# Optimization experiments

Measured on AMD Instinct MI355X. Metric: run time of the kernel, lower is better.

The kernel has to match this reference:

```python
import jax, jax.numpy as jnp
import numpy as np

B, C_IN, C_OUT, H, W = 4, 64, 64, 128, 128
N = 9  # 3x3 sampling points


def setup_inputs() -> dict:
    key = jax.random.key(0)
    k1, k2, k3, k4 = jax.random.split(key, 4)
    x = jax.random.normal(k1, (B, C_IN, H, W), jnp.float32)
    alpha = jax.random.normal(k2, (B, 1, H, W), jnp.float32)
    # kaiming_uniform(a=sqrt(5)) on (C_OUT, C_IN, 3, 3): bound = 1/sqrt(fan_in)
    fan_in = C_IN * 9
    bound = 1.0 / np.sqrt(fan_in)
    weight = jax.random.uniform(k3, (C_OUT, C_IN, 3, 3), jnp.float32, -bound, bound)
    bias = jax.random.uniform(k4, (C_OUT,), jnp.float32, -bound, bound)
    return {"x": x, "alpha": alpha, "weight": weight, "bias": bias}


def _forward(x, alpha, weight, bias):
    b, c, h, w = x.shape
    xp = jnp.pad(x, ((0, 0), (0, 0), (1, 1), (1, 1)))  # ZeroPad2d(1)
    hp, wp = h + 2, w + 2
    dt = x.dtype

    # kernel offsets, N index n = kx*3 + ky (kx slow)
    ks = jnp.arange(-1, 2, dtype=dt)
    pnx = jnp.repeat(ks, 3)  # [-1,-1,-1,0,0,0,1,1,1]
    pny = jnp.tile(ks, 3)    # [-1,0,1,-1,0,1,-1,0,1]

    cosA = jnp.cos(alpha)  # (b,1,h,w)
    sinA = jnp.sin(alpha)
    p0x = jnp.arange(1, h + 1, dtype=dt)[:, None]  # (h,1)
    p0y = jnp.arange(1, w + 1, dtype=dt)[None, :]  # (1,w)
    # note: original code multiplies each coord by (cos +/- sin) of alpha
    px = pnx[None, :, None, None] * (cosA + sinA) + p0x[None, None]  # (b,9,h,w)
    py = pny[None, :, None, None] * (cosA - sinA) + p0y[None, None]
    px = jnp.moveaxis(px, 1, -1)  # (b,h,w,9)
    py = jnp.moveaxis(py, 1, -1)

    fx, fy = jnp.floor(px), jnp.floor(py)  # detached in original (floor grad = 0)
    qx0 = jnp.clip(fx, 0, hp - 1)
    qx1 = jnp.clip(fx + 1, 0, hp - 1)
    qy0 = jnp.clip(fy, 0, wp - 1)
    qy1 = jnp.clip(fy + 1, 0, wp - 1)

    g_lt = (1 + (qx0 - px)) * (1 + (qy0 - py))
    g_rb = (1 - (qx1 - px)) * (1 - (qy1 - py))
    g_lb = (1 + (qx0 - px)) * (1 - (qy1 - py))
    g_rt = (1 - (qx1 - px)) * (1 + (qy0 - py))

    xf = xp.reshape(b, c, hp * wp)
    ix0, ix1 = qx0.astype(jnp.int32), qx1.astype(jnp.int32)
    iy0, iy1 = qy0.astype(jnp.int32), qy1.astype(jnp.int32)

    def gather(ix, iy):
        idx = (ix * wp + iy).reshape(b, -1)  # row-major flatten, like torch gather
        v = jax.vmap(lambda xb, ib: xb[:, ib])(xf, idx)  # (b,c,h*w*9)
        return v.reshape(b, c, h, w, N)

    emap = (g_lt[:, None] * gather(ix0, iy0)
            + g_rb[:, None] * gather(ix1, iy1)
            + g_lb[:, None] * gather(ix0, iy1)
            + g_rt[:, None] * gather(ix1, iy0))  # (b,c,h,w,9)

    # _reshape_x_offset: out[b,c, i*3+ky, j*3+kx] = emap[b,c,i,j, kx*3+ky]
    e = emap.reshape(b, c, h, w, 3, 3)              # (...,kx,ky)
    e = e.transpose(0, 1, 2, 5, 3, 4).reshape(b, c, 3 * h, 3 * w)

    # Dconv: central-difference weights, middle row = -(top + bottom)
    o, i = weight.shape[0], weight.shape[1]
    wr = weight.reshape(o, i, 9)
    r0, r2 = wr[:, :, 0:3], wr[:, :, 6:9]
    buf = jnp.concatenate([r0, -r0 - r2, r2], axis=-1).reshape(o, i, 3, 3)

    y = jax.lax.conv_general_dilated(
        e, buf, window_strides=(3, 3), padding='VALID',
        dimension_numbers=('NCHW', 'OIHW', 'NCHW'))
    return y + bias[None, :, None, None]


def reference(x, alpha, weight, bias):
    return _forward(x, alpha, weight, bias)
```

## Files before the change

### kernel.cpp

```cpp
#include <hip/hip_runtime.h>

#define CIN  64
#define COUT 64
#define Hn   128
#define Wn   128
#define HW   (Hn * Wn)
#define KDIM 576
#define WROW 1152
#define EROW 640

#define NRQ 5
#define NCQ 36
#define NCHUNKQ (NRQ * NCQ * 8)
#define TILE_BYTES (NCHUNKQ * 16)

typedef __attribute__((ext_vector_type(8))) short bf16x8;
typedef __attribute__((ext_vector_type(4))) float f32x4;
typedef __attribute__((ext_vector_type(2))) float f32x2;

__device__ __forceinline__ unsigned short f2bf(float f) {
    unsigned u = __float_as_uint(f);
    unsigned r = u + 0x7FFFu + ((u >> 16) & 1u);
    return (unsigned short)(r >> 16);
}
__device__ __forceinline__ unsigned pk2(float a, float b) {
    return (unsigned)f2bf(a) | ((unsigned)f2bf(b) << 16);
}
__device__ __forceinline__ unsigned pk2h(float a, float b) {
    unsigned ua = __float_as_uint(a) + 0x8000u;
    unsigned ub = __float_as_uint(b) + 0x8000u;
    return __builtin_amdgcn_perm(ub, ua, 0x07060302u);
}


__global__ __launch_bounds__(256) void prep_fused(
    const float* __restrict__ x, const float* __restrict__ weight,
    unsigned short* __restrict__ xt, unsigned short* __restrict__ Wtb2)
{
    __shared__ float fbuf[64][65];
    if (blockIdx.x >= 1024) {
        int e = (blockIdx.x - 1024) * 256 + threadIdx.x;
        if (e < COUT * KDIM) {
            int o = e / KDIM, k = e % KDIM;
            int n = k >> 6, c = k & 63;
            int u = n % 3, v = n / 3;
            float w0 = weight[((o * CIN + c) * 3 + 0) * 3 + v];
            float w2 = weight[((o * CIN + c) * 3 + 2) * 3 + v];
            float val = (u == 0) ? w0 : ((u == 1) ? (-w0 - w2) : w2);
            int s = c >> 5;
            int ce = c & 31;
            Wtb2[((n * 2 + s) * 64 + o) * 32 + ce] = f2bf(val);
        }
        return;
    }
    const int blk = blockIdx.x;
    const int b   = blk >> 8;
    const int rem = blk & 255;
    const int h   = rem >> 1;
    const int w0  = (rem & 1) << 6;
    const int t   = threadIdx.x;
    {
        int wq = t & 63, cq = t >> 6;
        const float* xp = x + ((size_t)(b * CIN + cq * 16) * Hn + h) * Wn + w0 + wq;
        #pragma unroll
        for (int r = 0; r < 16; ++r)
            fbuf[wq][cq * 16 + r] = xp[(size_t)r * HW];
    }
    __syncthreads();
    {
        int wq = t >> 2, q = t & 3;
        const float* row = &fbuf[wq][q * 16];
        uint4 d0, d1;
        d0.x = pk2(row[0],  row[1]);  d0.y = pk2(row[2],  row[3]);
        d0.z = pk2(row[4],  row[5]);  d0.w = pk2(row[6],  row[7]);
        d1.x = pk2(row[8],  row[9]);  d1.y = pk2(row[10], row[11]);
        d1.z = pk2(row[12], row[13]); d1.w = pk2(row[14], row[15]);
        unsigned short* op = xt + ((size_t)(b * Hn + h) * Wn + w0 + wq) * 64 + q * 16;
        *reinterpret_cast<uint4*>(op)     = d0;
        *reinterpret_cast<uint4*>(op + 8) = d1;
    }
}

template<int D>
__device__ __forceinline__ void axis_pts(float s, int base1, int org,
                                         int& l0, int& l1, float& w0, float& w1)
{
    if (D) {
        float p  = (float)D * s + (float)base1;
        float f  = floorf(p);
        float q0 = fminf(fmaxf(f,       0.f), 129.f);
        float q1 = fminf(fmaxf(f + 1.f, 0.f), 129.f);
        w0 = 1.f + (q0 - p);  w1 = 1.f - (q1 - p);
        int i0 = (int)q0, i1 = (int)q1;
        if (i0 < 1 || i0 > 128) w0 = 0.f;
        if (i1 < 1 || i1 > 128) w1 = 0.f;
        l0 = min(max(i0 - 1, 0), 127) - org;
        l1 = min(max(i1 - 1, 0), 127) - org;
    } else {
        l0 = base1 - 1 - org;  w0 = 1.f;
        l1 = l0;               w1 = 0.f;
    }
}

__device__ __forceinline__ void mkpt(int lr, int lc, int g16,
                                     unsigned& offL, unsigned& offH) {
    unsigned base = (unsigned)((lr * NCQ + lc) << 7);
    unsigned m    = ((unsigned)lc & 7u) << 4;
    offL = base + (((unsigned)g16) ^ m);
    offH = base + (((unsigned)(64 + g16)) ^ m);
}

template<int DX, int DY>
__device__ __forceinline__ void geoC(float s1, float s2, int i, int j0, int lpx,
        int g16, unsigned oL[4], unsigned oH[4], float gw[4])
{
    int r0, r1, c0, c1; float wx0, wx1, wy0, wy1;
    axis_pts<DX>(s1, i + 1,        i - 2,  r0, r1, wx0, wx1);
    axis_pts<DY>(s2, j0 + lpx + 1, j0 - 2, c0, c1, wy0, wy1);
    mkpt(r0, c0, g16, oL[0], oH[0]);  gw[0] = wx0 * wy0;
    mkpt(r0, c1, g16, oL[1], oH[1]);  gw[1] = wx0 * wy1;
    mkpt(r1, c0, g16, oL[2], oH[2]);  gw[2] = wx1 * wy0;
    mkpt(r1, c1, g16, oL[3], oH[3]);  gw[3] = wx1 * wy1;
}

template<int DX, int DY>
__device__ __forceinline__ void geoE(float s1, float s2, int i, int j0, int lpx,
        int g16, unsigned oL[2], unsigned oH[2], float gw[2])
{
    if (DX == 0) {
        int c0, c1; float wy0, wy1;
        axis_pts<DY>(s2, j0 + lpx + 1, j0 - 2, c0, c1, wy0, wy1);
        mkpt(2, c0, g16, oL[0], oH[0]);  gw[0] = wy0;
        mkpt(2, c1, g16, oL[1], oH[1]);  gw[1] = wy1;
    } else {
        int r0, r1; float wx0, wx1;
        axis_pts<DX>(s1, i + 1, i - 2, r0, r1, wx0, wx1);
        mkpt(r0, lpx + 2, g16, oL[0], oH[0]);  gw[0] = wx0;
        mkpt(r1, lpx + 2, g16, oL[1], oH[1]);  gw[1] = wx1;
    }
}

__device__ __forceinline__ f32x2 bfpair(unsigned u) {
    f32x2 r;
    r.x = __uint_as_float(u << 16);
    r.y = __uint_as_float(u & 0xFFFF0000u);
    return r;
}

__device__ __forceinline__ void fma16p(uint4 rl, uint4 rh, float gw,
                                       f32x2* v0, f32x2* v1) {
    const unsigned* u0 = reinterpret_cast<const unsigned*>(&rl);
    const unsigned* u1 = reinterpret_cast<const unsigned*>(&rh);
    f32x2 g2; g2.x = gw; g2.y = gw;
    #pragma unroll
    for (int q = 0; q < 4; ++q) {
        v0[q] = __builtin_elementwise_fma(g2, bfpair(u0[q]), v0[q]);
        v1[q] = __builtin_elementwise_fma(g2, bfpair(u1[q]), v1[q]);
    }
}

__device__ __forceinline__ bf16x8 packv2(const f32x2* v) {
    uint4 p;
    p.x = pk2h(v[0].x, v[0].y); p.y = pk2h(v[1].x, v[1].y);
    p.z = pk2h(v[2].x, v[2].y); p.w = pk2h(v[3].x, v[3].y);
    union { uint4 u; bf16x8 b; } cv; cv.u = p;
    return cv.b;
}

__global__ __launch_bounds__(256, 3) void ddconv_ws3(
    const unsigned short* __restrict__ xt, const float* __restrict__ alpha,
    const unsigned short* __restrict__ Wtb2, const float* __restrict__ bias,
    float* __restrict__ out)
{
    __shared__ __align__(16) char smem[40960];

    const int blk  = blockIdx.x;
    const int b    = blk >> 9;
    const int rem  = blk & 511;
    const int i    = rem >> 2;
    const int j0   = (rem & 3) << 5;
    const int t    = threadIdx.x;
    const int lane = t & 63;
    const int w    = t >> 6;
    const int llo  = lane & 15;
    const int g    = lane >> 4;
    const int g16  = g * 16;

    const char* xtb = (const char*)xt + (size_t)b * HW * 128;
    const char* wt2 = (const char*)Wtb2;
    const int arow  = llo * 64 + g16;

    char* tile = smem;
    uint4    sv[6];
    unsigned sla[6];
    {
        const char* sgp[6];
        #pragma unroll
        for (int k = 0; k < 6; ++k) {
            int q = t + k * 256;
            if (k == 5) q = min(q, NCHUNKQ - 1);
            int slot = q & 7;
            int rc   = q >> 3;
            int row  = rc / NCQ;
            int col  = rc - row * NCQ;
            int ru   = min(max(i - 2 + row, 0), 127);
            int cu   = min(max(j0 - 2 + col, 0), 127);
            sgp[k] = xtb + (size_t)(((ru << 7) + cu) << 7) + (slot << 4);
            sla[k] = ((unsigned)rc << 7) + (((unsigned)slot << 4) ^ (((unsigned)col & 7u) << 4));
        }
        #pragma unroll
        for (int k = 0; k < 6; ++k)
            sv[k] = *reinterpret_cast<const uint4*>(sgp[k]);
    }
    #pragma unroll
    for (int k = 0; k < 5; ++k)
        *reinterpret_cast<uint4*>(tile + sla[k]) = sv[k];
    if (t < NCHUNKQ - 5 * 256)
        *reinterpret_cast<uint4*>(tile + sla[5]) = sv[5];

    const int nn0 = (w==0)?0:(w==1)?2:(w==2)?6:8;
    const int nn1 = (w==0)?1:(w==1)?3:(w==2)?7:5;
    const int cs  = w >> 1;
    bf16x8 Ata[2][4], Atb[2][4], Ac0, Ac1;
    #pragma unroll
    for (int s = 0; s < 2; ++s)
      #pragma unroll
      for (int ot = 0; ot < 4; ++ot) {
        Ata[s][ot] = *reinterpret_cast<const bf16x8*>(wt2 + (nn0*2+s)*4096 + ot*1024 + arow);
        Atb[s][ot] = *reinterpret_cast<const bf16x8*>(wt2 + (nn1*2+s)*4096 + ot*1024 + arow);
      }
    Ac0 = *reinterpret_cast<const bf16x8*>(wt2 + (8+cs)*4096 + ((w&1)*2  )*1024 + arow);
    Ac1 = *reinterpret_cast<const bf16x8*>(wt2 + (8+cs)*4096 + ((w&1)*2+1)*1024 + arow);

    float* sAB = reinterpret_cast<float*>(smem + TILE_BYTES);
    if (t < 32) {
        float a = alpha[(b * Hn + i) * Wn + j0 + t];
        float sa, ca;
        sincosf(a, &sa, &ca);
        sAB[t]      = ca + sa;
        sAB[32 + t] = ca - sa;
    }

    f32x4 acc[2][4];
    #pragma unroll
    for (int pg = 0; pg < 2; ++pg)
      #pragma unroll
      for (int ot = 0; ot < 4; ++ot) acc[pg][ot] = (f32x4){0.f, 0.f, 0.f, 0.f};

    __syncthreads();

    float S1[2], S2[2];
    #pragma unroll
    for (int pg = 0; pg < 2; ++pg) {
        S1[pg] = sAB[pg * 16 + llo];
        S2[pg] = sAB[32 + pg * 16 + llo];
    }

    #pragma unroll
    for (int pg = 0; pg < 2; ++pg) {
        const int lpx = pg * 16 + llo;

        unsigned AL[4], AH[4], BL[2], BH[2];
        float    AG[4], BG[2];
        if (w == 0) {
            geoC<-1,-1>(S1[pg], S2[pg], i, j0, lpx, g16, AL, AH, AG);
            geoE<-1, 0>(S1[pg], S2[pg], i, j0, lpx, g16, BL, BH, BG);
        } else if (w == 1) {
            geoC<-1, 1>(S1[pg], S2[pg], i, j0, lpx, g16, AL, AH, AG);
            geoE< 0,-1>(S1[pg], S2[pg], i, j0, lpx, g16, BL, BH, BG);
        } else if (w == 2) {
            geoC< 1,-1>(S1[pg], S2[pg], i, j0, lpx, g16, AL, AH, AG);
            geoE< 1, 0>(S1[pg], S2[pg], i, j0, lpx, g16, BL, BH, BG);
        } else {
            geoC< 1, 1>(S1[pg], S2[pg], i, j0, lpx, g16, AL, AH, AG);
            geoE< 0, 1>(S1[pg], S2[pg], i, j0, lpx, g16, BL, BH, BG);
        }
        unsigned cb    = (unsigned)((2 * NCQ + lpx + 2) << 7);
        unsigned cm    = ((unsigned)(lpx + 2) & 7u) << 4;
        unsigned cAddr = cb + ((cs ? (unsigned)(64 + g16) : (unsigned)g16) ^ cm);

        uint4 La[4], Ha[4];
        #pragma unroll
        for (int p = 0; p < 4; ++p) {
            La[p] = *reinterpret_cast<const uint4*>(tile + AL[p]);
            Ha[p] = *reinterpret_cast<const uint4*>(tile + AH[p]);
        }
        uint4 Lb[2], Hb[2];
        #pragma unroll
        for (int p = 0; p < 2; ++p) {
            Lb[p] = *reinterpret_cast<const uint4*>(tile + BL[p]);
            Hb[p] = *reinterpret_cast<const uint4*>(tile + BH[p]);
        }
        bf16x8 bc = *reinterpret_cast<const bf16x8*>(tile + cAddr);

        f32x2 v0[4], v1[4];
        #pragma unroll
        for (int q = 0; q < 4; ++q) { v0[q] = (f32x2){0.f,0.f}; v1[q] = (f32x2){0.f,0.f}; }
        #pragma unroll
        for (int p = 0; p < 4; ++p) fma16p(La[p], Ha[p], AG[p], v0, v1);
        bf16x8 bA0 = packv2(v0), bA1 = packv2(v1);

        f32x2 u0[4], u1[4];
        #pragma unroll
        for (int q = 0; q < 4; ++q) { u0[q] = (f32x2){0.f,0.f}; u1[q] = (f32x2){0.f,0.f}; }
        #pragma unroll
        for (int p = 0; p < 2; ++p) fma16p(Lb[p], Hb[p], BG[p], u0, u1);
        bf16x8 bB0 = packv2(u0), bB1 = packv2(u1);

        #pragma unroll
        for (int ot = 0; ot < 4; ++ot) {
            acc[pg][ot] = __builtin_amdgcn_mfma_f32_16x16x32_bf16(Ata[0][ot], bA0, acc[pg][ot], 0, 0, 0);
            acc[pg][ot] = __builtin_amdgcn_mfma_f32_16x16x32_bf16(Ata[1][ot], bA1, acc[pg][ot], 0, 0, 0);
            acc[pg][ot] = __builtin_amdgcn_mfma_f32_16x16x32_bf16(Atb[0][ot], bB0, acc[pg][ot], 0, 0, 0);
            acc[pg][ot] = __builtin_amdgcn_mfma_f32_16x16x32_bf16(Atb[1][ot], bB1, acc[pg][ot], 0, 0, 0);
        }
        if (w & 1) {
            acc[pg][2] = __builtin_amdgcn_mfma_f32_16x16x32_bf16(Ac0, bc, acc[pg][2], 0, 0, 0);
            acc[pg][3] = __builtin_amdgcn_mfma_f32_16x16x32_bf16(Ac1, bc, acc[pg][3], 0, 0, 0);
        } else {
            acc[pg][0] = __builtin_amdgcn_mfma_f32_16x16x32_bf16(Ac0, bc, acc[pg][0], 0, 0, 0);
            acc[pg][1] = __builtin_amdgcn_mfma_f32_16x16x32_bf16(Ac1, bc, acc[pg][1], 0, 0, 0);
        }
    }

    __syncthreads();
    #pragma unroll
    for (int pg = 0; pg < 2; ++pg)
      #pragma unroll
      for (int ot = 0; ot < 4; ++ot)
        *reinterpret_cast<f32x4*>(smem + ((pg*256 + w*64 + lane)*80) + ot*16) = acc[pg][ot];
    __syncthreads();
    {
        const int eq = w;
        #pragma unroll
        for (int pg = 0; pg < 2; ++pg) {
            f32x4 s = (f32x4){0.f, 0.f, 0.f, 0.f};
            #pragma unroll
            for (int ww = 0; ww < 4; ++ww)
                s += *reinterpret_cast<const f32x4*>(smem + ((pg*256 + ww*64 + lane)*80) + eq*16);
            int jj = j0 + pg * 16 + llo;
            float* ob = out + (size_t)b * COUT * HW + (size_t)i * Wn + jj;
            #pragma unroll
            for (int r = 0; r < 4; ++r) {
                int o = eq * 16 + g * 4 + r;
                ob[(size_t)o * HW] = s[r] + bias[o];
            }
        }
    }
}


__global__ void prep_weights(const float* __restrict__ weight,
                             unsigned short* __restrict__ Wtb) {
    int e = blockIdx.x * 256 + threadIdx.x;
    if (e >= COUT * KDIM) return;
    int o = e / KDIM, k = e % KDIM;
    int n = k >> 6, c = k & 63;
    int u = n % 3, v = n / 3;
    float w0 = weight[((o * CIN + c) * 3 + 0) * 3 + v];
    float w2 = weight[((o * CIN + c) * 3 + 2) * 3 + v];
    float val = (u == 0) ? w0 : ((u == 1) ? (-w0 - w2) : w2);
    Wtb[o * KDIM + k] = f2bf(val);
}

template<int DX, int DY>
__device__ __forceinline__ void gatherG(const float* __restrict__ xb,
    float s1, float s2, int i, int jj, int klocal,
    char* myrow, unsigned swz, int c0s, int c1s)
{
    int ix0 = 0, ix1 = 0; float wx0 = 1.f, wx1 = 0.f;
    if (DX != 0) {
        float px = (float)DX * s1 + (float)(i + 1);
        float fx = floorf(px);
        float qx0 = fminf(fmaxf(fx, 0.f), 129.f);
        float qx1 = fminf(fmaxf(fx + 1.f, 0.f), 129.f);
        wx0 = 1.f + (qx0 - px); wx1 = 1.f - (qx1 - px);
        ix0 = (int)qx0; ix1 = (int)qx1;
    } else { ix0 = i + 1; }
    int iy0 = 0, iy1 = 0; float wy0 = 1.f, wy1 = 0.f;
    if (DY != 0) {
        float py = (float)DY * s2 + (float)(jj + 1);
        float fy = floorf(py);
        float qy0 = fminf(fmaxf(fy, 0.f), 129.f);
        float qy1 = fminf(fmaxf(fy + 1.f, 0.f), 129.f);
        wy0 = 1.f + (qy0 - py); wy1 = 1.f - (qy1 - py);
        iy0 = (int)qy0; iy1 = (int)qy1;
    } else { iy0 = jj + 1; }

    constexpr int NX = (DX ? 2 : 1), NY = (DY ? 2 : 1), NT = NX * NY;
    unsigned idx[NT]; float g[NT];
    const int   ixs[2] = { ix0, ix1 };  const float wxs[2] = { wx0, wx1 };
    const int   iys[2] = { iy0, iy1 };  const float wys[2] = { wy0, wy1 };
    #pragma unroll
    for (int xi = 0; xi < NX; ++xi)
      #pragma unroll
      for (int yi = 0; yi < NY; ++yi) {
        int ix = ixs[xi], iy = iys[yi];
        bool ok = (ix >= 1) && (ix <= Hn) && (iy >= 1) && (iy <= Wn);
        int cx = min(max(ix, 1), Hn) - 1;
        int cy = min(max(iy, 1), Wn) - 1;
        idx[xi * NY + yi] = (unsigned)(cx * Wn + cy);
        g[xi * NY + yi]   = ok ? wxs[xi] * wys[yi] : 0.f;
      }
    for (int c0 = c0s; c0 < c1s; c0 += 8) {
        float v[8];
        #pragma unroll
        for (int cc = 0; cc < 8; ++cc) {
            unsigned coff = (unsigned)(c0 + cc) * HW;
            float acc2 = 0.f;
            #pragma unroll
            for (int tp = 0; tp < NT; ++tp)
                acc2 = fmaf(g[tp], xb[coff + idx[tp]], acc2);
            v[cc] = acc2;
        }
        uint4 d;
        d.x = pk2(v[0], v[1]); d.y = pk2(v[2], v[3]);
        d.z = pk2(v[4], v[5]); d.w = pk2(v[6], v[7]);
        unsigned addr = (unsigned)(klocal + c0) * 2u;
        *reinterpret_cast<uint4*>(myrow + (addr ^ swz)) = d;
    }
}

template<int KS>
__device__ __forceinline__ void mfma_phase(const char* emap,
    const unsigned short* __restrict__ Wtb,
    int w, int lane, int passbyte, f32x4 acc[4])
{
    const int llo = lane & 15, lhi = lane >> 4;
    const unsigned prow = (unsigned)(w * 16 + llo);
    const unsigned psw  = (prow & 7u) << 4;
    const char* erow = emap + prow * EROW;
    const char* wtb  = (const char*)Wtb + passbyte + lhi * 16;
    #pragma unroll
    for (int s = 0; s < KS; ++s) {
        unsigned kb = (unsigned)(s * 64 + lhi * 16);
        bf16x8 bf = *reinterpret_cast<const bf16x8*>(erow + (kb ^ psw));
        #pragma unroll
        for (int ot = 0; ot < 4; ++ot) {
            const char* ap = wtb + (ot * 16 + llo) * WROW + s * 64;
            bf16x8 af = *reinterpret_cast<const bf16x8*>(ap);
            acc[ot] = __builtin_amdgcn_mfma_f32_16x16x32_bf16(af, bf, acc[ot], 0, 0, 0);
        }
    }
}

__global__ __launch_bounds__(256, 3) void ddconv_mfma(
    const float* __restrict__ x, const float* __restrict__ alpha,
    const unsigned short* __restrict__ Wtb, const float* __restrict__ bias,
    float* __restrict__ out)
{
    __shared__ __align__(16) char emap[64 * EROW];
    const int blk  = blockIdx.x;
    const int b    = blk >> 8;
    const int rem  = blk & 255;
    const int i    = rem >> 1;
    const int j0   = (rem & 1) << 6;
    const int t    = threadIdx.x;
    const int lane = t & 63;
    const int w    = t >> 6;
    const int jj   = j0 + lane;
    const float* xb = x + (size_t)b * CIN * HW;
    float a = alpha[(b * Hn + i) * Wn + jj];
    float sa, ca;
    sincosf(a, &sa, &ca);
    const float s1 = ca + sa, s2 = ca - sa;
    char* myrow = emap + lane * EROW;
    const unsigned swz = (unsigned)((lane & 7) << 4);
    f32x4 acc[4];
    #pragma unroll
    for (int ot = 0; ot < 4; ++ot) acc[ot] = (f32x4){0.f, 0.f, 0.f, 0.f};
    if (w == 0)      { gatherG<-1,-1>(xb, s1, s2, i, jj,   0, myrow, swz,  0, 48); }
    else if (w == 1) { gatherG<-1,-1>(xb, s1, s2, i, jj,   0, myrow, swz, 48, 64);
                       gatherG<-1, 0>(xb, s1, s2, i, jj,  64, myrow, swz,  0, 64); }
    else if (w == 2) { gatherG<-1, 1>(xb, s1, s2, i, jj, 128, myrow, swz,  0, 48); }
    else             { gatherG<-1, 1>(xb, s1, s2, i, jj, 128, myrow, swz, 48, 64);
                       gatherG< 0,-1>(xb, s1, s2, i, jj, 192, myrow, swz,  0, 64); }
    __syncthreads();
    mfma_phase<8>(emap, Wtb, w, lane, 0, acc);
    __syncthreads();
    if (w == 0)      { gatherG< 1,-1>(xb, s1, s2, i, jj, 128, myrow, swz,  0, 56); }
    else if (w == 1) { gatherG< 1,-1>(xb, s1, s2, i, jj, 128, myrow, swz, 56, 64);
                       gatherG< 1, 1>(xb, s1, s2, i, jj, 256, myrow, swz,  0, 48); }
    else if (w == 2) { gatherG< 1, 1>(xb, s1, s2, i, jj, 256, myrow, swz, 48, 64);
                       gatherG< 0, 1>(xb, s1, s2, i, jj,  64, myrow, swz,  0, 64); }
    else             { gatherG< 1, 0>(xb, s1, s2, i, jj, 192, myrow, swz,  0, 64);
                       gatherG< 0, 0>(xb, s1, s2, i, jj,   0, myrow, swz,  0, 64); }
    __syncthreads();
    mfma_phase<10>(emap, Wtb, w, lane, 512, acc);
    const int llo = lane & 15, lhi = lane >> 4;
    float* ob = out + (size_t)b * COUT * HW + (size_t)i * Wn + j0 + w * 16 + llo;
    #pragma unroll
    for (int ot = 0; ot < 4; ++ot)
      #pragma unroll
      for (int r = 0; r < 4; ++r) {
        int o = ot * 16 + lhi * 4 + r;
        ob[(size_t)o * HW] = acc[ot][r] + bias[o];
      }
}


extern "C" void kernel_launch(void* const* d_in, const int* in_sizes, int n_in,
                              void* d_out, int out_size, void* d_ws, size_t ws_size,
                              hipStream_t stream) {
    const float* x      = (const float*)d_in[0];
    const float* alpha  = (const float*)d_in[1];
    const float* weight = (const float*)d_in[2];
    const float* bias   = (const float*)d_in[3];
    float* out = (float*)d_out;

    const size_t WT_BYTES = (size_t)COUT * KDIM * 2;
    const size_t XT_BYTES = (size_t)4 * HW * CIN * 2;

    if (ws_size >= WT_BYTES + XT_BYTES) {
        unsigned short* Wtb2 = (unsigned short*)d_ws;
        unsigned short* xt   = (unsigned short*)((char*)d_ws + WT_BYTES);
        prep_fused<<<1168, 256, 0, stream>>>(x, weight, xt, Wtb2);
        ddconv_ws3<<<4 * Hn * (Wn / 32), 256, 0, stream>>>(xt, alpha, Wtb2, bias, out);
    } else {
        unsigned short* Wtb = (unsigned short*)d_ws;
        prep_weights<<<(COUT * KDIM + 255) / 256, 256, 0, stream>>>(weight, Wtb);
        ddconv_mfma<<<4 * Hn * (Wn / 64), 256, 0, stream>>>(x, alpha, Wtb, bias, out);
    }
}
```

Baseline: 36.41 us.

## Store input tile in shared memory pre-expanded to fp32 even/odd halves

The input tile in shared memory now holds each bf16 pair pre-split into two 32-bit words, low element shifted and high element masked. The split happens once at staging time instead of at every bilinear-sample read. The sampling loop reads fp32-ready words directly and software-pipelines the loads of the next corner against the current FMAs. The cost is twice the LDS tile size and twice the LDS read traffic, and the higher LDS footprint (about 46KB per block) may cut the number of resident blocks below the 3 requested by launch bounds.

```diff
diff --git a/kernel.cpp b/kernel.cpp
--- a/kernel.cpp
+++ b/kernel.cpp
@@ -12,7 +12,7 @@
 #define NRQ 5
 #define NCQ 36
 #define NCHUNKQ (NRQ * NCQ * 8)
-#define TILE_BYTES (NCHUNKQ * 16)
+#define TILE_BYTES (NCHUNKQ * 32)
 
 typedef __attribute__((ext_vector_type(8))) short bf16x8;
 typedef __attribute__((ext_vector_type(4))) float f32x4;
@@ -104,7 +104,7 @@
 
 __device__ __forceinline__ void mkpt(int lr, int lc, int g16,
                                      unsigned& offL, unsigned& offH) {
-    unsigned base = (unsigned)((lr * NCQ + lc) << 7);
+    unsigned base = (unsigned)((lr * NCQ + lc) << 8);
     unsigned m    = ((unsigned)lc & 7u) << 4;
     offL = base + (((unsigned)g16) ^ m);
     offH = base + (((unsigned)(64 + g16)) ^ m);
@@ -140,29 +140,22 @@
     }
 }
 
-__device__ __forceinline__ f32x2 bfpair(unsigned u) {
-    f32x2 r;
-    r.x = __uint_as_float(u << 16);
-    r.y = __uint_as_float(u & 0xFFFF0000u);
-    return r;
-}
-
-__device__ __forceinline__ void fma16p(uint4 rl, uint4 rh, float gw,
-                                       f32x2* v0, f32x2* v1) {
-    const unsigned* u0 = reinterpret_cast<const unsigned*>(&rl);
-    const unsigned* u1 = reinterpret_cast<const unsigned*>(&rh);
-    f32x2 g2; g2.x = gw; g2.y = gw;
-    #pragma unroll
-    for (int q = 0; q < 4; ++q) {
-        v0[q] = __builtin_elementwise_fma(g2, bfpair(u0[q]), v0[q]);
-        v1[q] = __builtin_elementwise_fma(g2, bfpair(u1[q]), v1[q]);
-    }
-}
-
-__device__ __forceinline__ bf16x8 packv2(const f32x2* v) {
+__device__ __forceinline__ f32x2 asf2(unsigned a, unsigned b) {
+    f32x2 r; r.x = __uint_as_float(a); r.y = __uint_as_float(b); return r;
+}
+
+__device__ __forceinline__ void fma8s(uint4 LQ, uint4 HQ, f32x2 g2,
+                                      f32x2* E, f32x2* O) {
+    E[0] = __builtin_elementwise_fma(g2, asf2(LQ.x, LQ.y), E[0]);
+    E[1] = __builtin_elementwise_fma(g2, asf2(LQ.z, LQ.w), E[1]);
+    O[0] = __builtin_elementwise_fma(g2, asf2(HQ.x, HQ.y), O[0]);
+    O[1] = __builtin_elementwise_fma(g2, asf2(HQ.z, HQ.w), O[1]);
+}
+
+__device__ __forceinline__ bf16x8 packv2s(const f32x2* E, const f32x2* O) {
     uint4 p;
-    p.x = pk2h(v[0].x, v[0].y); p.y = pk2h(v[1].x, v[1].y);
-    p.z = pk2h(v[2].x, v[2].y); p.w = pk2h(v[3].x, v[3].y);
+    p.x = pk2h(E[0].x, O[0].x); p.y = pk2h(E[0].y, O[0].y);
+    p.z = pk2h(E[1].x, O[1].x); p.w = pk2h(E[1].y, O[1].y);
     union { uint4 u; bf16x8 b; } cv; cv.u = p;
     return cv.b;
 }
@@ -172,7 +165,7 @@
     const unsigned short* __restrict__ Wtb2, const float* __restrict__ bias,
     float* __restrict__ out)
 {
-    __shared__ __align__(16) char smem[40960];
+    __shared__ __align__(16) char smem[46336];
 
     const int blk  = blockIdx.x;
     const int b    = blk >> 9;
@@ -206,17 +199,24 @@
             int ru   = min(max(i - 2 + row, 0), 127);
             int cu   = min(max(j0 - 2 + col, 0), 127);
             sgp[k] = xtb + (size_t)(((ru << 7) + cu) << 7) + (slot << 4);
-            sla[k] = ((unsigned)rc << 7) + (((unsigned)slot << 4) ^ (((unsigned)col & 7u) << 4));
+            sla[k] = ((unsigned)rc << 8) + (((unsigned)slot << 4) ^ (((unsigned)col & 7u) << 4));
         }
         #pragma unroll
         for (int k = 0; k < 6; ++k)
             sv[k] = *reinterpret_cast<const uint4*>(sgp[k]);
     }
     #pragma unroll
-    for (int k = 0; k < 5; ++k)
-        *reinterpret_cast<uint4*>(tile + sla[k]) = sv[k];
-    if (t < NCHUNKQ - 5 * 256)
-        *reinterpret_cast<uint4*>(tile + sla[5]) = sv[5];
+    for (int k = 0; k < 6; ++k) {
+        if (k == 5 && t >= NCHUNKQ - 5 * 256) break;
+        uint4 v = sv[k];
+        uint4 lq, hq;
+        lq.x = v.x << 16;          lq.y = v.y << 16;
+        lq.z = v.z << 16;          lq.w = v.w << 16;
+        hq.x = v.x & 0xFFFF0000u;  hq.y = v.y & 0xFFFF0000u;
+        hq.z = v.z & 0xFFFF0000u;  hq.w = v.w & 0xFFFF0000u;
+        *reinterpret_cast<uint4*>(tile + sla[k])       = lq;
+        *reinterpret_cast<uint4*>(tile + sla[k] + 128) = hq;
+    }
 
     const int nn0 = (w==0)?0:(w==1)?2:(w==2)?6:8;
     const int nn1 = (w==0)?1:(w==1)?3:(w==2)?7:5;
@@ -255,6 +255,8 @@
         S1[pg] = sAB[pg * 16 + llo];
         S2[pg] = sAB[32 + pg * 16 + llo];
     }
+
+    #define LDT(o) (*reinterpret_cast<const uint4*>(tile + (o)))
 
     #pragma unroll
     for (int pg = 0; pg < 2; ++pg) {
@@ -275,37 +277,64 @@
             geoC< 1, 1>(S1[pg], S2[pg], i, j0, lpx, g16, AL, AH, AG);
             geoE< 0, 1>(S1[pg], S2[pg], i, j0, lpx, g16, BL, BH, BG);
         }
-        unsigned cb    = (unsigned)((2 * NCQ + lpx + 2) << 7);
+        unsigned cb    = (unsigned)((2 * NCQ + lpx + 2) << 8);
         unsigned cm    = ((unsigned)(lpx + 2) & 7u) << 4;
         unsigned cAddr = cb + ((cs ? (unsigned)(64 + g16) : (unsigned)g16) ^ cm);
 
-        uint4 La[4], Ha[4];
+        f32x2 vE[2], vO[2], wE[2], wO[2];
+        #pragma unroll
+        for (int q = 0; q < 2; ++q) {
+            vE[q] = (f32x2){0.f,0.f}; vO[q] = (f32x2){0.f,0.f};
+            wE[q] = (f32x2){0.f,0.f}; wO[q] = (f32x2){0.f,0.f};
+        }
+
+        uint4 tl0 = LDT(AL[0]), th0 = LDT(AL[0] + 128);
+        uint4 tl1 = LDT(AH[0]), th1 = LDT(AH[0] + 128);
         #pragma unroll
         for (int p = 0; p < 4; ++p) {
-            La[p] = *reinterpret_cast<const uint4*>(tile + AL[p]);
-            Ha[p] = *reinterpret_cast<const uint4*>(tile + AH[p]);
-        }
-        uint4 Lb[2], Hb[2];
-        #pragma unroll
-        for (int p = 0; p < 2; ++p) {
-            Lb[p] = *reinterpret_cast<const uint4*>(tile + BL[p]);
-            Hb[p] = *reinterpret_cast<const uint4*>(tile + BH[p]);
-        }
-        bf16x8 bc = *reinterpret_cast<const bf16x8*>(tile + cAddr);
-
-        f32x2 v0[4], v1[4];
-        #pragma unroll
-        for (int q = 0; q < 4; ++q) { v0[q] = (f32x2){0.f,0.f}; v1[q] = (f32x2){0.f,0.f}; }
-        #pragma unroll
-        for (int p = 0; p < 4; ++p) fma16p(La[p], Ha[p], AG[p], v0, v1);
-        bf16x8 bA0 = packv2(v0), bA1 = packv2(v1);
-
-        f32x2 u0[4], u1[4];
-        #pragma unroll
-        for (int q = 0; q < 4; ++q) { u0[q] = (f32x2){0.f,0.f}; u1[q] = (f32x2){0.f,0.f}; }
-        #pragma unroll
-        for (int p = 0; p < 2; ++p) fma16p(Lb[p], Hb[p], BG[p], u0, u1);
-        bf16x8 bB0 = packv2(u0), bB1 = packv2(u1);
+            uint4 nl0, nh0, nl1, nh1;
+            if (p < 3) {
+                nl0 = LDT(AL[p+1]); nh0 = LDT(AL[p+1] + 128);
+                nl1 = LDT(AH[p+1]); nh1 = LDT(AH[p+1] + 128);
+            }
+            f32x2 g2; g2.x = AG[p]; g2.y = AG[p];
+            fma8s(tl0, th0, g2, vE, vO);
+            fma8s(tl1, th1, g2, wE, wO);
+            if (p < 3) { tl0 = nl0; th0 = nh0; tl1 = nl1; th1 = nh1; }
+        }
+        bf16x8 bA0 = packv2s(vE, vO), bA1 = packv2s(wE, wO);
+
+        f32x2 uE[2], uO[2], tE[2], tO[2];
+        #pragma unroll
+        for (int q = 0; q < 2; ++q) {
+            uE[q] = (f32x2){0.f,0.f}; uO[q] = (f32x2){0.f,0.f};
+            tE[q] = (f32x2){0.f,0.f}; tO[q] = (f32x2){0.f,0.f};
+        }
+        {
+            uint4 el0 = LDT(BL[0]), eh0 = LDT(BL[0] + 128);
+            uint4 el1 = LDT(BH[0]), eh1 = LDT(BH[0] + 128);
+            uint4 fl0 = LDT(BL[1]), fh0 = LDT(BL[1] + 128);
+            uint4 fl1 = LDT(BH[1]), fh1 = LDT(BH[1] + 128);
+            f32x2 g2; g2.x = BG[0]; g2.y = BG[0];
+            fma8s(el0, eh0, g2, uE, uO);
+            fma8s(el1, eh1, g2, tE, tO);
+            g2.x = BG[1]; g2.y = BG[1];
+            fma8s(fl0, fh0, g2, uE, uO);
+            fma8s(fl1, fh1, g2, tE, tO);
+        }
+        bf16x8 bB0 = packv2s(uE, uO), bB1 = packv2s(tE, tO);
+
+        bf16x8 bc;
+        {
+            uint4 cl = LDT(cAddr), ch = LDT(cAddr + 128);
+            uint4 cp;
+            cp.x = __builtin_amdgcn_perm(ch.x, cl.x, 0x07060302u);
+            cp.y = __builtin_amdgcn_perm(ch.y, cl.y, 0x07060302u);
+            cp.z = __builtin_amdgcn_perm(ch.z, cl.z, 0x07060302u);
+            cp.w = __builtin_amdgcn_perm(ch.w, cl.w, 0x07060302u);
+            union { uint4 u; bf16x8 b; } cv; cv.u = cp;
+            bc = cv.b;
+        }
 
         #pragma unroll
         for (int ot = 0; ot < 4; ++ot) {
@@ -322,6 +351,7 @@
             acc[pg][1] = __builtin_amdgcn_mfma_f32_16x16x32_bf16(Ac1, bc, acc[pg][1], 0, 0, 0);
         }
     }
+    #undef LDT
 
     __syncthreads();
     #pragma unroll
```

Result: slower. 37.83 us (+3.9%).

## Retile conv blocks to 2x16 pixels to shrink the halo tile

Applied to the files above, without the earlier changes.

Each block now computes a 2-row by 16-column output patch instead of 1 row by 32 columns, and the shared-memory tile becomes 6x20 pixels instead of 5x36. This cuts the halo pixels loaded per block, so there are fewer global loads and LDS stores, and it also lowers LDS use. Geometry helpers now take explicit row and column origins. In exchange, output stores per row are only 16 floats wide, so they are less coalesced.

```diff
diff --git a/kernel.cpp b/kernel.cpp
--- a/kernel.cpp
+++ b/kernel.cpp
@@ -9,8 +9,8 @@
 #define WROW 1152
 #define EROW 640
 
-#define NRQ 5
-#define NCQ 36
+#define NRQ 6
+#define NCQ 20
 #define NCHUNKQ (NRQ * NCQ * 8)
 #define TILE_BYTES (NCHUNKQ * 16)
 
@@ -111,12 +111,12 @@
 }
 
 template<int DX, int DY>
-__device__ __forceinline__ void geoC(float s1, float s2, int i, int j0, int lpx,
-        int g16, unsigned oL[4], unsigned oH[4], float gw[4])
+__device__ __forceinline__ void geoC(float s1, float s2, int ipx, int iorg,
+        int jpx, int jorg, int g16, unsigned oL[4], unsigned oH[4], float gw[4])
 {
     int r0, r1, c0, c1; float wx0, wx1, wy0, wy1;
-    axis_pts<DX>(s1, i + 1,        i - 2,  r0, r1, wx0, wx1);
-    axis_pts<DY>(s2, j0 + lpx + 1, j0 - 2, c0, c1, wy0, wy1);
+    axis_pts<DX>(s1, ipx + 1, iorg, r0, r1, wx0, wx1);
+    axis_pts<DY>(s2, jpx + 1, jorg, c0, c1, wy0, wy1);
     mkpt(r0, c0, g16, oL[0], oH[0]);  gw[0] = wx0 * wy0;
     mkpt(r0, c1, g16, oL[1], oH[1]);  gw[1] = wx0 * wy1;
     mkpt(r1, c0, g16, oL[2], oH[2]);  gw[2] = wx1 * wy0;
@@ -124,19 +124,19 @@
 }
 
 template<int DX, int DY>
-__device__ __forceinline__ void geoE(float s1, float s2, int i, int j0, int lpx,
-        int g16, unsigned oL[2], unsigned oH[2], float gw[2])
+__device__ __forceinline__ void geoE(float s1, float s2, int ipx, int iorg,
+        int jpx, int jorg, int g16, unsigned oL[2], unsigned oH[2], float gw[2])
 {
     if (DX == 0) {
         int c0, c1; float wy0, wy1;
-        axis_pts<DY>(s2, j0 + lpx + 1, j0 - 2, c0, c1, wy0, wy1);
-        mkpt(2, c0, g16, oL[0], oH[0]);  gw[0] = wy0;
-        mkpt(2, c1, g16, oL[1], oH[1]);  gw[1] = wy1;
+        axis_pts<DY>(s2, jpx + 1, jorg, c0, c1, wy0, wy1);
+        mkpt(ipx - iorg, c0, g16, oL[0], oH[0]);  gw[0] = wy0;
+        mkpt(ipx - iorg, c1, g16, oL[1], oH[1]);  gw[1] = wy1;
     } else {
         int r0, r1; float wx0, wx1;
-        axis_pts<DX>(s1, i + 1, i - 2, r0, r1, wx0, wx1);
-        mkpt(r0, lpx + 2, g16, oL[0], oH[0]);  gw[0] = wx0;
-        mkpt(r1, lpx + 2, g16, oL[1], oH[1]);  gw[1] = wx1;
+        axis_pts<DX>(s1, ipx + 1, iorg, r0, r1, wx0, wx1);
+        mkpt(r0, jpx - jorg, g16, oL[0], oH[0]);  gw[0] = wx0;
+        mkpt(r1, jpx - jorg, g16, oL[1], oH[1]);  gw[1] = wx1;
     }
 }
 
@@ -177,46 +177,47 @@
     const int blk  = blockIdx.x;
     const int b    = blk >> 9;
     const int rem  = blk & 511;
-    const int i    = rem >> 2;
-    const int j0   = (rem & 3) << 5;
+    const int i0   = (rem >> 3) << 1;
+    const int j0   = (rem & 7) << 4;
     const int t    = threadIdx.x;
     const int lane = t & 63;
     const int w    = t >> 6;
     const int llo  = lane & 15;
     const int g    = lane >> 4;
     const int g16  = g * 16;
+    const int iorg = i0 - 2, jorg = j0 - 2;
 
     const char* xtb = (const char*)xt + (size_t)b * HW * 128;
     const char* wt2 = (const char*)Wtb2;
     const int arow  = llo * 64 + g16;
 
     char* tile = smem;
-    uint4    sv[6];
-    unsigned sla[6];
+    uint4    sv[4];
+    unsigned sla[4];
     {
-        const char* sgp[6];
-        #pragma unroll
-        for (int k = 0; k < 6; ++k) {
+        const char* sgp[4];
+        #pragma unroll
+        for (int k = 0; k < 4; ++k) {
             int q = t + k * 256;
-            if (k == 5) q = min(q, NCHUNKQ - 1);
+            if (k == 3) q = min(q, NCHUNKQ - 1);
             int slot = q & 7;
             int rc   = q >> 3;
             int row  = rc / NCQ;
             int col  = rc - row * NCQ;
-            int ru   = min(max(i - 2 + row, 0), 127);
-            int cu   = min(max(j0 - 2 + col, 0), 127);
+            int ru   = min(max(iorg + row, 0), 127);
+            int cu   = min(max(jorg + col, 0), 127);
             sgp[k] = xtb + (size_t)(((ru << 7) + cu) << 7) + (slot << 4);
             sla[k] = ((unsigned)rc << 7) + (((unsigned)slot << 4) ^ (((unsigned)col & 7u) << 4));
         }
         #pragma unroll
-        for (int k = 0; k < 6; ++k)
+        for (int k = 0; k < 4; ++k)
             sv[k] = *reinterpret_cast<const uint4*>(sgp[k]);
     }
     #pragma unroll
-    for (int k = 0; k < 5; ++k)
+    for (int k = 0; k < 3; ++k)
         *reinterpret_cast<uint4*>(tile + sla[k]) = sv[k];
-    if (t < NCHUNKQ - 5 * 256)
-        *reinterpret_cast<uint4*>(tile + sla[5]) = sv[5];
+    if (t < NCHUNKQ - 3 * 256)
+        *reinterpret_cast<uint4*>(tile + sla[3]) = sv[3];
 
     const int nn0 = (w==0)?0:(w==1)?2:(w==2)?6:8;
     const int nn1 = (w==0)?1:(w==1)?3:(w==2)?7:5;
@@ -234,7 +235,7 @@
 
     float* sAB = reinterpret_cast<float*>(smem + TILE_BYTES);
     if (t < 32) {
-        float a = alpha[(b * Hn + i) * Wn + j0 + t];
+        float a = alpha[(b * Hn + i0 + (t >> 4)) * Wn + j0 + (t & 15)];
         float sa, ca;
         sincosf(a, &sa, &ca);
         sAB[t]      = ca + sa;
@@ -258,25 +259,27 @@
 
     #pragma unroll
     for (int pg = 0; pg < 2; ++pg) {
-        const int lpx = pg * 16 + llo;
+        const int ipx = i0 + pg;
+        const int jpx = j0 + llo;
 
         unsigned AL[4], AH[4], BL[2], BH[2];
         float    AG[4], BG[2];
         if (w == 0) {
-            geoC<-1,-1>(S1[pg], S2[pg], i, j0, lpx, g16, AL, AH, AG);
-            geoE<-1, 0>(S1[pg], S2[pg], i, j0, lpx, g16, BL, BH, BG);
+            geoC<-1,-1>(S1[pg], S2[pg], ipx, iorg, jpx, jorg, g16, AL, AH, AG);
+            geoE<-1, 0>(S1[pg], S2[pg], ipx, iorg, jpx, jorg, g16, BL, BH, BG);
         } else if (w == 1) {
-            geoC<-1, 1>(S1[pg], S2[pg], i, j0, lpx, g16, AL, AH, AG);
-            geoE< 0,-1>(S1[pg], S2[pg], i, j0, lpx, g16, BL, BH, BG);
+            geoC<-1, 1>(S1[pg], S2[pg], ipx, iorg, jpx, jorg, g16, AL, AH, AG);
+            geoE< 0,-1>(S1[pg], S2[pg], ipx, iorg, jpx, jorg, g16, BL, BH, BG);
         } else if (w == 2) {
-            geoC< 1,-1>(S1[pg], S2[pg], i, j0, lpx, g16, AL, AH, AG);
-            geoE< 1, 0>(S1[pg], S2[pg], i, j0, lpx, g16, BL, BH, BG);
+            geoC< 1,-1>(S1[pg], S2[pg], ipx, iorg, jpx, jorg, g16, AL, AH, AG);
+            geoE< 1, 0>(S1[pg], S2[pg], ipx, iorg, jpx, jorg, g16, BL, BH, BG);
         } else {
-            geoC< 1, 1>(S1[pg], S2[pg], i, j0, lpx, g16, AL, AH, AG);
-            geoE< 0, 1>(S1[pg], S2[pg], i, j0, lpx, g16, BL, BH, BG);
-        }
-        unsigned cb    = (unsigned)((2 * NCQ + lpx + 2) << 7);
-        unsigned cm    = ((unsigned)(lpx + 2) & 7u) << 4;
+            geoC< 1, 1>(S1[pg], S2[pg], ipx, iorg, jpx, jorg, g16, AL, AH, AG);
+            geoE< 0, 1>(S1[pg], S2[pg], ipx, iorg, jpx, jorg, g16, BL, BH, BG);
+        }
+        const int lcc  = jpx - jorg;
+        unsigned cb    = (unsigned)((((ipx - iorg) * NCQ) + lcc) << 7);
+        unsigned cm    = ((unsigned)lcc & 7u) << 4;
         unsigned cAddr = cb + ((cs ? (unsigned)(64 + g16) : (unsigned)g16) ^ cm);
 
         uint4 La[4], Ha[4];
@@ -338,8 +341,7 @@
             #pragma unroll
             for (int ww = 0; ww < 4; ++ww)
                 s += *reinterpret_cast<const f32x4*>(smem + ((pg*256 + ww*64 + lane)*80) + eq*16);
-            int jj = j0 + pg * 16 + llo;
-            float* ob = out + (size_t)b * COUT * HW + (size_t)i * Wn + jj;
+            float* ob = out + (size_t)b * COUT * HW + (size_t)(i0 + pg) * Wn + j0 + llo;
             #pragma unroll
             for (int r = 0; r < 4; ++r) {
                 int o = eq * 16 + g * 4 + r;
@@ -515,7 +517,7 @@
         unsigned short* Wtb2 = (unsigned short*)d_ws;
         unsigned short* xt   = (unsigned short*)((char*)d_ws + WT_BYTES);
         prep_fused<<<1168, 256, 0, stream>>>(x, weight, xt, Wtb2);
-        ddconv_ws3<<<4 * Hn * (Wn / 32), 256, 0, stream>>>(xt, alpha, Wtb2, bias, out);
+        ddconv_ws3<<<4 * (Hn / 2) * (Wn / 16), 256, 0, stream>>>(xt, alpha, Wtb2, bias, out);
     } else {
         unsigned short* Wtb = (unsigned short*)d_ws;
         prep_weights<<<(COUT * KDIM + 255) / 256, 256, 0, stream>>>(weight, Wtb);
```

New measurement: 32.41 us. 11.0% less time.
